# Kernel tuning notes

Hardware: AMD Instinct MI355X
Metric: run time of the kernel (lower is better)

Reference implementation:

```python
import jax, jax.numpy as jnp
import numpy as np

B, NP, NT = 16, 4096, 77
QD, CD, H, DH = 512, 768, 8, 64
INNER = H * DH


def setup_inputs() -> dict:
    key = jax.random.key(0)
    ks = jax.random.split(key, 8)
    s = 0.02
    return {
        "x": jax.random.normal(ks[0], (B, NP, QD), jnp.float32),
        "context": jax.random.normal(ks[1], (B, NT, CD), jnp.float32),
        "mask": jnp.ones((B, NP, NT), jnp.int32),
        "Wq": jax.random.normal(ks[2], (QD, INNER), jnp.float32) * s,
        "Wk": jax.random.normal(ks[3], (CD, INNER), jnp.float32) * s,
        "Wv": jax.random.normal(ks[4], (CD, INNER), jnp.float32) * s,
        "Wo": jax.random.normal(ks[5], (INNER, QD), jnp.float32) * s,
        "bo": jnp.zeros((QD,), jnp.float32),
    }


def reference(x, context, mask, Wq, Wk, Wv, Wo, bo):
    scale = 1.0 / jnp.sqrt(jnp.asarray(DH, x.dtype))
    # projections -> (B, H, N, DH)
    q = (x @ Wq).reshape(B, NP, H, DH).transpose(0, 2, 1, 3)
    k = (context @ Wk).reshape(B, NT, H, DH).transpose(0, 2, 1, 3)
    v = (context @ Wv).reshape(B, NT, H, DH).transpose(0, 2, 1, 3)
    # scores (B, H, NP, NT)
    attn = jnp.einsum("bhqd,bhkd->bhqk", q, k) * scale
    attn = jnp.where(mask[:, None, :, :] == 0, -jnp.inf, attn)
    attn = jax.nn.softmax(attn, axis=-1)
    out = jnp.einsum("bhqk,bhkd->bhqd", attn, v)
    out = out.transpose(0, 2, 1, 3).reshape(B, NP, INNER)
    return out @ Wo + bo
```

## Files before the change

kernel.cpp:

```cpp
#include <hip/hip_runtime.h>


typedef _Float16 half_t;
typedef _Float16 half8 __attribute__((ext_vector_type(8)));
typedef float f32x4 __attribute__((ext_vector_type(4)));
typedef unsigned int u32;

#define NB 16
#define NP 4096
#define NT 77
#define NTP 96
#define QD 512
#define CD 768
#define NH 8
#define DH 64
#define INNER 512
#define MKV (NB * NT)

__device__ __forceinline__ void stage16(const void* g, void* l) {
    __builtin_amdgcn_global_load_lds((const __attribute__((address_space(1))) u32*)g,
                                     (__attribute__((address_space(3))) u32*)l, 16, 0, 0);
}

__device__ __forceinline__ f32x4 mfma16(half8 a, half8 b, f32x4 c) {
    return __builtin_amdgcn_mfma_f32_16x16x32_f16(a, b, c, 0, 0, 0);
}

__global__ __launch_bounds__(256) void kTrans2(const float* __restrict__ in0,
                                               const float* __restrict__ in1,
                                               half_t* __restrict__ out0,
                                               half_t* __restrict__ out1,
                                               int K, int N) {
    const float* in = blockIdx.z ? in1 : in0;
    half_t* out = blockIdx.z ? out1 : out0;
    __shared__ float tile[32][33];
    int tx = threadIdx.x & 31, ty = threadIdx.x >> 5;
    int kb = blockIdx.y * 32, nb = blockIdx.x * 32;
    for (int r = ty; r < 32; r += 8)
        tile[r][tx] = in[(size_t)(kb + r) * N + nb + tx];
    __syncthreads();
    for (int r = ty; r < 32; r += 8)
        out[(size_t)(nb + r) * K + kb + tx] = (half_t)tile[tx][r];
}

__global__ __launch_bounds__(256) void kKVproj(const float* __restrict__ Ctx,
                                               const half_t* __restrict__ WkT,
                                               const half_t* __restrict__ WvT,
                                               half_t* __restrict__ Kp,
                                               half_t* __restrict__ VTp) {
    __shared__ alignas(16) half_t As[64 * 64];
    __shared__ alignas(16) half_t Bs[128 * 64];
    const int t = threadIdx.x, w = t >> 6, lane = t & 63;
    const int c0 = lane & 15, q4 = lane >> 4;
    const int rx = c0 & 7;
    const int m0 = blockIdx.y * 64;
    const int n0g = blockIdx.x * 128;
    const int z = n0g >= 512;
    const int n0 = n0g - z * 512;
    const half_t* WT = z ? WvT : WkT;

    f32x4 acc[4][2] = {};
    for (int k0 = 0; k0 < CD; k0 += 64) {
        for (int q = 0; q < 2; ++q) {
            int c = q * 256 + t;
            int row = c >> 3, ch = c & 7;
            int gr = m0 + row; if (gr > MKV - 1) gr = MKV - 1;
            const float* src = Ctx + (size_t)gr * CD + k0 + ch * 8;
            f32x4 f0 = *(const f32x4*)src;
            f32x4 f1 = *(const f32x4*)(src + 4);
            half8 hv;
            for (int e = 0; e < 4; ++e) { hv[e] = (half_t)f0[e]; hv[4 + e] = (half_t)f1[e]; }
            *(half8*)&As[row * 64 + ((ch ^ (row & 7)) * 8)] = hv;
        }
        for (int q = 0; q < 4; ++q) {
            int c = q * 256 + t;
            int row = c >> 3, k8 = c & 7;
            stage16(WT + (size_t)(n0 + row) * CD + k0 + (k8 ^ (row & 7)) * 8, &Bs[c * 8]);
        }
        __syncthreads();
        for (int ks = 0; ks < 2; ++ks) {
            int ch = ks * 4 + q4;
            int cx = (ch ^ rx) * 8;
            half8 a[4], b[2];
            for (int i = 0; i < 4; ++i)
                a[i] = *(const half8*)&As[(16 * i + c0) * 64 + cx];
            for (int j = 0; j < 2; ++j)
                b[j] = *(const half8*)&Bs[(w * 32 + 16 * j + c0) * 64 + cx];
            for (int i = 0; i < 4; ++i)
                for (int j = 0; j < 2; ++j)
                    acc[i][j] = mfma16(a[i], b[j], acc[i][j]);
        }
        __syncthreads();
    }
    for (int i = 0; i < 4; ++i)
        for (int j = 0; j < 2; ++j)
            for (int r = 0; r < 4; ++r) {
                int row = m0 + 16 * i + q4 * 4 + r;
                if (row >= MKV) continue;
                int col = n0 + w * 32 + 16 * j + c0;
                int b = row / NT, tt = row - b * NT;
                int h = col >> 6, d = col & 63;
                half_t v = (half_t)acc[i][j][r];
                if (!z) Kp[(((size_t)b * NH + h) * NTP + tt) * DH + d] = v;
                else    VTp[(((size_t)b * NH + h) * DH + d) * NTP + tt] = v;
            }
}

__global__ __launch_bounds__(256) void kQproj(const float* __restrict__ X,
                                              const half_t* __restrict__ WqT,
                                              half_t* __restrict__ Q) {
    __shared__ alignas(16) half_t As[128 * 64];
    __shared__ alignas(16) half_t Bs[128 * 64];
    const int t = threadIdx.x, w = t >> 6, lane = t & 63;
    const int c0 = lane & 15, q4 = lane >> 4;
    const int rx = c0 & 7;
    const int wm = w & 1, wn = w >> 1;
    const int bid = blockIdx.x;
    const int wid = (bid & 7) * 256 + (bid >> 3);
    const int m0 = (wid >> 2) * 128, n0 = (wid & 3) * 128;

    f32x4 acc[4][4] = {};
    for (int k0 = 0; k0 < QD; k0 += 64) {
        for (int q = 0; q < 4; ++q) {
            int c = q * 256 + t;
            int row = c >> 3, ch = c & 7;
            const float* src = X + (size_t)(m0 + row) * QD + k0 + ch * 8;
            f32x4 f0 = *(const f32x4*)src;
            f32x4 f1 = *(const f32x4*)(src + 4);
            half8 hv;
            for (int e = 0; e < 4; ++e) { hv[e] = (half_t)f0[e]; hv[4 + e] = (half_t)f1[e]; }
            *(half8*)&As[row * 64 + ((ch ^ (row & 7)) * 8)] = hv;
        }
        for (int q = 0; q < 4; ++q) {
            int c = q * 256 + t;
            int row = c >> 3, k8 = c & 7;
            stage16(WqT + (size_t)(n0 + row) * QD + k0 + (k8 ^ (row & 7)) * 8, &Bs[c * 8]);
        }
        __syncthreads();
        for (int ks = 0; ks < 2; ++ks) {
            int cx = ((ks * 4 + q4) ^ rx) * 8;
            half8 a[4];
            for (int i = 0; i < 4; ++i)
                a[i] = *(const half8*)&As[(wm * 64 + 16 * i + c0) * 64 + cx];
            for (int j = 0; j < 4; ++j) {
                half8 bv = *(const half8*)&Bs[(wn * 64 + 16 * j + c0) * 64 + cx];
                for (int i = 0; i < 4; ++i)
                    acc[i][j] = mfma16(a[i], bv, acc[i][j]);
            }
        }
        __syncthreads();
    }
    for (int i = 0; i < 4; ++i)
        for (int j = 0; j < 4; ++j)
            for (int r = 0; r < 4; ++r) {
                int row = m0 + wm * 64 + 16 * i + q4 * 4 + r;
                int col = n0 + wn * 64 + 16 * j + c0;
                Q[(size_t)row * INNER + col] = (half_t)acc[i][j][r];
            }
}

__global__ __launch_bounds__(256) void kAttn(half_t* __restrict__ Q,
                                             const half_t* __restrict__ Kp,
                                             const half_t* __restrict__ VTp,
                                             const int* __restrict__ mask) {
    __shared__ alignas(16) half_t Qs[128 * 104];
    __shared__ alignas(16) half_t Ks[NTP * 72];
    __shared__ alignas(16) half_t VTs[DH * 104];
    const int t = threadIdx.x, w = t >> 6, lane = t & 63;
    const int c0 = lane & 15, q4 = lane >> 4;
    const int qt = blockIdx.x, h = blockIdx.y, b = blockIdx.z;
    const int q0 = qt * 128;
    const size_t qbase = ((size_t)b * NP + q0) * INNER + h * DH;

    for (int q = 0; q < 4; ++q) {
        int c = q * 256 + t, m = c >> 3, k8 = (c & 7) * 8;
        *(uint4*)&Qs[m * 104 + k8] = *(const uint4*)(Q + qbase + (size_t)m * INNER + k8);
    }
    const half_t* Kh = Kp + ((size_t)b * NH + h) * NTP * DH;
    for (int q = 0; q < 3; ++q) {
        int c = q * 256 + t, r = c >> 3, k8 = (c & 7) * 8;
        *(uint4*)&Ks[r * 72 + k8] = *(const uint4*)(Kh + r * DH + k8);
    }
    const half_t* Vh = VTp + ((size_t)b * NH + h) * DH * NTP;
    for (int q = 0; q < 3; ++q) {
        int c = q * 256 + t, r = c / 12, t8 = (c % 12) * 8;
        *(uint4*)&VTs[r * 104 + t8] = *(const uint4*)(Vh + r * NTP + t8);
    }
    __syncthreads();

    const int r0 = w * 32;
    f32x4 sacc[2][6] = {};
    for (int ks = 0; ks < 2; ++ks) {
        half8 a0 = *(const half8*)&Qs[(r0 + c0) * 104 + ks * 32 + q4 * 8];
        half8 a1 = *(const half8*)&Qs[(r0 + 16 + c0) * 104 + ks * 32 + q4 * 8];
        for (int j = 0; j < 6; ++j) {
            half8 bv = *(const half8*)&Ks[(16 * j + c0) * 72 + ks * 32 + q4 * 8];
            sacc[0][j] = mfma16(a0, bv, sacc[0][j]);
            sacc[1][j] = mfma16(a1, bv, sacc[1][j]);
        }
    }

    for (int i = 0; i < 2; ++i)
        for (int r = 0; r < 4; ++r) {
            int qrow = r0 + 16 * i + q4 * 4 + r;
            const int* mrow = mask + ((size_t)b * NP + q0 + qrow) * NT;
            float sv[6];
            for (int j = 0; j < 6; ++j) {
                int tt = 16 * j + c0;
                float s = sacc[i][j][r] * 0.125f;
                bool valid = (tt < NT) && (mrow[tt < NT ? tt : NT - 1] != 0);
                sv[j] = valid ? s : -1e30f;
            }
            float mx = sv[0];
            for (int j = 1; j < 6; ++j) mx = fmaxf(mx, sv[j]);
            for (int d = 1; d < 16; d <<= 1) mx = fmaxf(mx, __shfl_xor(mx, d));
            float pv[6], sum = 0.f;
            for (int j = 0; j < 6; ++j) { pv[j] = __expf(sv[j] - mx); sum += pv[j]; }
            for (int d = 1; d < 16; d <<= 1) sum += __shfl_xor(sum, d);
            float inv = 1.0f / sum;
            for (int j = 0; j < 6; ++j)
                Qs[qrow * 104 + 16 * j + c0] = (half_t)(pv[j] * inv);
        }

    f32x4 oacc[2][4] = {};
    for (int ks = 0; ks < 3; ++ks) {
        half8 a0 = *(const half8*)&Qs[(r0 + c0) * 104 + ks * 32 + q4 * 8];
        half8 a1 = *(const half8*)&Qs[(r0 + 16 + c0) * 104 + ks * 32 + q4 * 8];
        for (int j = 0; j < 4; ++j) {
            half8 bv = *(const half8*)&VTs[(16 * j + c0) * 104 + ks * 32 + q4 * 8];
            oacc[0][j] = mfma16(a0, bv, oacc[0][j]);
            oacc[1][j] = mfma16(a1, bv, oacc[1][j]);
        }
    }
    for (int i = 0; i < 2; ++i)
        for (int j = 0; j < 4; ++j)
            for (int r = 0; r < 4; ++r) {
                int qrow = r0 + 16 * i + q4 * 4 + r;
                int d = 16 * j + c0;
                Q[qbase + (size_t)qrow * INNER + d] = (half_t)oacc[2 > 1 ? i : i][j][r];
            }
}

__global__ __launch_bounds__(256) void kOproj(const half_t* __restrict__ AO,
                                              const half_t* __restrict__ WoT,
                                              const float* __restrict__ bo,
                                              float* __restrict__ out) {
    __shared__ alignas(16) half_t As[128 * 64];
    __shared__ alignas(16) half_t Bs[128 * 64];
    const int t = threadIdx.x, w = t >> 6, lane = t & 63;
    const int c0 = lane & 15, q4 = lane >> 4;
    const int rx = c0 & 7;
    const int wm = w & 1, wn = w >> 1;
    const int bid = blockIdx.x;
    const int wid = (bid & 7) * 256 + (bid >> 3);
    const int m0 = (wid >> 2) * 128, n0 = (wid & 3) * 128;

    float bj[4];
    for (int j = 0; j < 4; ++j) bj[j] = bo[n0 + wn * 64 + 16 * j + c0];

    f32x4 acc[4][4] = {};
    for (int k0 = 0; k0 < INNER; k0 += 64) {
        for (int q = 0; q < 4; ++q) {
            int c = q * 256 + t;
            int row = c >> 3, k8 = c & 7;
            stage16(AO + (size_t)(m0 + row) * INNER + k0 + (k8 ^ (row & 7)) * 8, &As[c * 8]);
        }
        for (int q = 0; q < 4; ++q) {
            int c = q * 256 + t;
            int row = c >> 3, k8 = c & 7;
            stage16(WoT + (size_t)(n0 + row) * INNER + k0 + (k8 ^ (row & 7)) * 8, &Bs[c * 8]);
        }
        __syncthreads();
        for (int ks = 0; ks < 2; ++ks) {
            int cx = ((ks * 4 + q4) ^ rx) * 8;
            half8 a[4];
            for (int i = 0; i < 4; ++i)
                a[i] = *(const half8*)&As[(wm * 64 + 16 * i + c0) * 64 + cx];
            for (int j = 0; j < 4; ++j) {
                half8 bv = *(const half8*)&Bs[(wn * 64 + 16 * j + c0) * 64 + cx];
                for (int i = 0; i < 4; ++i)
                    acc[i][j] = mfma16(a[i], bv, acc[i][j]);
            }
        }
        __syncthreads();
    }
    for (int i = 0; i < 4; ++i)
        for (int j = 0; j < 4; ++j)
            for (int r = 0; r < 4; ++r) {
                int row = m0 + wm * 64 + 16 * i + q4 * 4 + r;
                int col = n0 + wn * 64 + 16 * j + c0;
                out[(size_t)row * QD + col] = acc[i][j][r] + bj[j];
            }
}

extern "C" void kernel_launch(void* const* d_in, const int* in_sizes, int n_in,
                              void* d_out, int out_size, void* d_ws, size_t ws_size,
                              hipStream_t stream) {
    const float* x   = (const float*)d_in[0];
    const float* ctx = (const float*)d_in[1];
    const int*   msk = (const int*)d_in[2];
    const float* Wq  = (const float*)d_in[3];
    const float* Wk  = (const float*)d_in[4];
    const float* Wv  = (const float*)d_in[5];
    const float* Wo  = (const float*)d_in[6];
    const float* bo  = (const float*)d_in[7];
    float* out = (float*)d_out;

    half_t* Qws = (half_t*)d_ws;
    half_t* WqT = Qws + (size_t)NB * NP * INNER;
    half_t* WoT = WqT + (size_t)QD * INNER;
    half_t* WkT = WoT + (size_t)INNER * QD;
    half_t* WvT = WkT + (size_t)INNER * CD;
    half_t* Kp  = WvT + (size_t)INNER * CD;
    half_t* VTp = Kp + (size_t)NB * NH * NTP * DH;

    kTrans2<<<dim3(INNER / 32, QD / 32, 2), 256, 0, stream>>>(Wq, Wo, WqT, WoT, QD, INNER);
    kTrans2<<<dim3(INNER / 32, CD / 32, 2), 256, 0, stream>>>(Wk, Wv, WkT, WvT, CD, INNER);
    hipMemsetAsync(Kp, 0, (size_t)NB * NH * (NTP * DH + DH * NTP) * sizeof(half_t), stream);
    kKVproj<<<dim3(8, 20), 256, 0, stream>>>(ctx, WkT, WvT, Kp, VTp);
    kQproj<<<dim3(2048), 256, 0, stream>>>(x, WqT, Qws);
    kAttn<<<dim3(NP / 128, NH, NB), 256, 0, stream>>>(Qws, Kp, VTp, msk);
    kOproj<<<dim3(2048), 256, 0, stream>>>(Qws, WoT, bo, out);
}
```

Baseline: 407.4 us.

## Double-buffer LDS tiles in projection GEMMs and raise MFMA wave priority in attention

Converts the K/V, Q and output projection GEMMs to a double-buffered LDS pipeline. The next k-tile's global loads (register prefetch plus fp16 convert for the fp32 activations, direct-to-LDS for the weights) are issued before the MFMAs on the current tile, so load latency can overlap compute and only one barrier per iteration remains. It also wraps the attention kernel's MFMA loops in s_setprio to favor matrix-issuing waves. The cost is doubled LDS use (64 KB for the 128x128 GEMMs), which may lower occupancy, plus extra prefetch registers.

```diff
diff --git a/kernel.cpp b/kernel.cpp
--- a/kernel.cpp
+++ b/kernel.cpp
@@ -48,8 +48,8 @@
                                                const half_t* __restrict__ WvT,
                                                half_t* __restrict__ Kp,
                                                half_t* __restrict__ VTp) {
-    __shared__ alignas(16) half_t As[64 * 64];
-    __shared__ alignas(16) half_t Bs[128 * 64];
+    __shared__ alignas(16) half_t As[2][64 * 64];
+    __shared__ alignas(16) half_t Bs[2][128 * 64];
     const int t = threadIdx.x, w = t >> 6, lane = t & 63;
     const int c0 = lane & 15, q4 = lane >> 4;
     const int rx = c0 & 7;
@@ -59,38 +59,54 @@
     const int n0 = n0g - z * 512;
     const half_t* WT = z ? WvT : WkT;
 
-    f32x4 acc[4][2] = {};
-    for (int k0 = 0; k0 < CD; k0 += 64) {
+    f32x4 pf[2][2];
+    auto issueA = [&](int k0) {
         for (int q = 0; q < 2; ++q) {
             int c = q * 256 + t;
             int row = c >> 3, ch = c & 7;
             int gr = m0 + row; if (gr > MKV - 1) gr = MKV - 1;
             const float* src = Ctx + (size_t)gr * CD + k0 + ch * 8;
-            f32x4 f0 = *(const f32x4*)src;
-            f32x4 f1 = *(const f32x4*)(src + 4);
+            pf[q][0] = *(const f32x4*)src;
+            pf[q][1] = *(const f32x4*)(src + 4);
+        }
+    };
+    auto writeA = [&](half_t* dst) {
+        for (int q = 0; q < 2; ++q) {
+            int c = q * 256 + t;
+            int row = c >> 3, ch = c & 7;
             half8 hv;
-            for (int e = 0; e < 4; ++e) { hv[e] = (half_t)f0[e]; hv[4 + e] = (half_t)f1[e]; }
-            *(half8*)&As[row * 64 + ((ch ^ (row & 7)) * 8)] = hv;
-        }
+            for (int e = 0; e < 4; ++e) { hv[e] = (half_t)pf[q][0][e]; hv[4 + e] = (half_t)pf[q][1][e]; }
+            *(half8*)&dst[row * 64 + ((ch ^ (row & 7)) * 8)] = hv;
+        }
+    };
+    auto stageB = [&](int k0, half_t* dst) {
         for (int q = 0; q < 4; ++q) {
             int c = q * 256 + t;
             int row = c >> 3, k8 = c & 7;
-            stage16(WT + (size_t)(n0 + row) * CD + k0 + (k8 ^ (row & 7)) * 8, &Bs[c * 8]);
-        }
-        __syncthreads();
+            stage16(WT + (size_t)(n0 + row) * CD + k0 + (k8 ^ (row & 7)) * 8, &dst[c * 8]);
+        }
+    };
+
+    f32x4 acc[4][2] = {};
+    issueA(0); stageB(0, Bs[0]); writeA(As[0]);
+    __syncthreads();
+    int cb = 0;
+    for (int it = 0; it < 12; ++it) {
+        if (it < 11) { issueA((it + 1) * 64); stageB((it + 1) * 64, Bs[cb ^ 1]); }
         for (int ks = 0; ks < 2; ++ks) {
-            int ch = ks * 4 + q4;
-            int cx = (ch ^ rx) * 8;
+            int cx = ((ks * 4 + q4) ^ rx) * 8;
             half8 a[4], b[2];
             for (int i = 0; i < 4; ++i)
-                a[i] = *(const half8*)&As[(16 * i + c0) * 64 + cx];
+                a[i] = *(const half8*)&As[cb][(16 * i + c0) * 64 + cx];
             for (int j = 0; j < 2; ++j)
-                b[j] = *(const half8*)&Bs[(w * 32 + 16 * j + c0) * 64 + cx];
+                b[j] = *(const half8*)&Bs[cb][(w * 32 + 16 * j + c0) * 64 + cx];
             for (int i = 0; i < 4; ++i)
                 for (int j = 0; j < 2; ++j)
                     acc[i][j] = mfma16(a[i], b[j], acc[i][j]);
         }
+        if (it < 11) writeA(As[cb ^ 1]);
         __syncthreads();
+        cb ^= 1;
     }
     for (int i = 0; i < 4; ++i)
         for (int j = 0; j < 2; ++j)
@@ -109,8 +125,8 @@
 __global__ __launch_bounds__(256) void kQproj(const float* __restrict__ X,
                                               const half_t* __restrict__ WqT,
                                               half_t* __restrict__ Q) {
-    __shared__ alignas(16) half_t As[128 * 64];
-    __shared__ alignas(16) half_t Bs[128 * 64];
+    __shared__ alignas(16) half_t As[2][128 * 64];
+    __shared__ alignas(16) half_t Bs[2][128 * 64];
     const int t = threadIdx.x, w = t >> 6, lane = t & 63;
     const int c0 = lane & 15, q4 = lane >> 4;
     const int rx = c0 & 7;
@@ -119,36 +135,53 @@
     const int wid = (bid & 7) * 256 + (bid >> 3);
     const int m0 = (wid >> 2) * 128, n0 = (wid & 3) * 128;
 
-    f32x4 acc[4][4] = {};
-    for (int k0 = 0; k0 < QD; k0 += 64) {
+    f32x4 pf[4][2];
+    auto issueA = [&](int k0) {
         for (int q = 0; q < 4; ++q) {
             int c = q * 256 + t;
             int row = c >> 3, ch = c & 7;
             const float* src = X + (size_t)(m0 + row) * QD + k0 + ch * 8;
-            f32x4 f0 = *(const f32x4*)src;
-            f32x4 f1 = *(const f32x4*)(src + 4);
+            pf[q][0] = *(const f32x4*)src;
+            pf[q][1] = *(const f32x4*)(src + 4);
+        }
+    };
+    auto writeA = [&](half_t* dst) {
+        for (int q = 0; q < 4; ++q) {
+            int c = q * 256 + t;
+            int row = c >> 3, ch = c & 7;
             half8 hv;
-            for (int e = 0; e < 4; ++e) { hv[e] = (half_t)f0[e]; hv[4 + e] = (half_t)f1[e]; }
-            *(half8*)&As[row * 64 + ((ch ^ (row & 7)) * 8)] = hv;
-        }
+            for (int e = 0; e < 4; ++e) { hv[e] = (half_t)pf[q][0][e]; hv[4 + e] = (half_t)pf[q][1][e]; }
+            *(half8*)&dst[row * 64 + ((ch ^ (row & 7)) * 8)] = hv;
+        }
+    };
+    auto stageB = [&](int k0, half_t* dst) {
         for (int q = 0; q < 4; ++q) {
             int c = q * 256 + t;
             int row = c >> 3, k8 = c & 7;
-            stage16(WqT + (size_t)(n0 + row) * QD + k0 + (k8 ^ (row & 7)) * 8, &Bs[c * 8]);
-        }
-        __syncthreads();
+            stage16(WqT + (size_t)(n0 + row) * QD + k0 + (k8 ^ (row & 7)) * 8, &dst[c * 8]);
+        }
+    };
+
+    f32x4 acc[4][4] = {};
+    issueA(0); stageB(0, Bs[0]); writeA(As[0]);
+    __syncthreads();
+    int cb = 0;
+    for (int it = 0; it < 8; ++it) {
+        if (it < 7) { issueA((it + 1) * 64); stageB((it + 1) * 64, Bs[cb ^ 1]); }
         for (int ks = 0; ks < 2; ++ks) {
             int cx = ((ks * 4 + q4) ^ rx) * 8;
             half8 a[4];
             for (int i = 0; i < 4; ++i)
-                a[i] = *(const half8*)&As[(wm * 64 + 16 * i + c0) * 64 + cx];
+                a[i] = *(const half8*)&As[cb][(wm * 64 + 16 * i + c0) * 64 + cx];
             for (int j = 0; j < 4; ++j) {
-                half8 bv = *(const half8*)&Bs[(wn * 64 + 16 * j + c0) * 64 + cx];
+                half8 bv = *(const half8*)&Bs[cb][(wn * 64 + 16 * j + c0) * 64 + cx];
                 for (int i = 0; i < 4; ++i)
                     acc[i][j] = mfma16(a[i], bv, acc[i][j]);
             }
         }
+        if (it < 7) writeA(As[cb ^ 1]);
         __syncthreads();
+        cb ^= 1;
     }
     for (int i = 0; i < 4; ++i)
         for (int j = 0; j < 4; ++j)
@@ -190,6 +223,7 @@
 
     const int r0 = w * 32;
     f32x4 sacc[2][6] = {};
+    __builtin_amdgcn_s_setprio(1);
     for (int ks = 0; ks < 2; ++ks) {
         half8 a0 = *(const half8*)&Qs[(r0 + c0) * 104 + ks * 32 + q4 * 8];
         half8 a1 = *(const half8*)&Qs[(r0 + 16 + c0) * 104 + ks * 32 + q4 * 8];
@@ -199,6 +233,7 @@
             sacc[1][j] = mfma16(a1, bv, sacc[1][j]);
         }
     }
+    __builtin_amdgcn_s_setprio(0);
 
     for (int i = 0; i < 2; ++i)
         for (int r = 0; r < 4; ++r) {
@@ -223,6 +258,7 @@
         }
 
     f32x4 oacc[2][4] = {};
+    __builtin_amdgcn_s_setprio(1);
     for (int ks = 0; ks < 3; ++ks) {
         half8 a0 = *(const half8*)&Qs[(r0 + c0) * 104 + ks * 32 + q4 * 8];
         half8 a1 = *(const half8*)&Qs[(r0 + 16 + c0) * 104 + ks * 32 + q4 * 8];
@@ -232,12 +268,13 @@
             oacc[1][j] = mfma16(a1, bv, oacc[1][j]);
         }
     }
+    __builtin_amdgcn_s_setprio(0);
     for (int i = 0; i < 2; ++i)
         for (int j = 0; j < 4; ++j)
             for (int r = 0; r < 4; ++r) {
                 int qrow = r0 + 16 * i + q4 * 4 + r;
                 int d = 16 * j + c0;
-                Q[qbase + (size_t)qrow * INNER + d] = (half_t)oacc[2 > 1 ? i : i][j][r];
+                Q[qbase + (size_t)qrow * INNER + d] = (half_t)oacc[i][j][r];
             }
 }
 
@@ -245,8 +282,8 @@
                                               const half_t* __restrict__ WoT,
                                               const float* __restrict__ bo,
                                               float* __restrict__ out) {
-    __shared__ alignas(16) half_t As[128 * 64];
-    __shared__ alignas(16) half_t Bs[128 * 64];
+    __shared__ alignas(16) half_t As[2][128 * 64];
+    __shared__ alignas(16) half_t Bs[2][128 * 64];
     const int t = threadIdx.x, w = t >> 6, lane = t & 63;
     const int c0 = lane & 15, q4 = lane >> 4;
     const int rx = c0 & 7;
@@ -258,31 +295,38 @@
     float bj[4];
     for (int j = 0; j < 4; ++j) bj[j] = bo[n0 + wn * 64 + 16 * j + c0];
 
+    auto stageAB = [&](int k0, half_t* dA, half_t* dB) {
+        for (int q = 0; q < 4; ++q) {
+            int c = q * 256 + t;
+            int row = c >> 3, k8 = c & 7;
+            stage16(AO + (size_t)(m0 + row) * INNER + k0 + (k8 ^ (row & 7)) * 8, &dA[c * 8]);
+        }
+        for (int q = 0; q < 4; ++q) {
+            int c = q * 256 + t;
+            int row = c >> 3, k8 = c & 7;
+            stage16(WoT + (size_t)(n0 + row) * INNER + k0 + (k8 ^ (row & 7)) * 8, &dB[c * 8]);
+        }
+    };
+
     f32x4 acc[4][4] = {};
-    for (int k0 = 0; k0 < INNER; k0 += 64) {
-        for (int q = 0; q < 4; ++q) {
-            int c = q * 256 + t;
-            int row = c >> 3, k8 = c & 7;
-            stage16(AO + (size_t)(m0 + row) * INNER + k0 + (k8 ^ (row & 7)) * 8, &As[c * 8]);
-        }
-        for (int q = 0; q < 4; ++q) {
-            int c = q * 256 + t;
-            int row = c >> 3, k8 = c & 7;
-            stage16(WoT + (size_t)(n0 + row) * INNER + k0 + (k8 ^ (row & 7)) * 8, &Bs[c * 8]);
-        }
-        __syncthreads();
+    stageAB(0, As[0], Bs[0]);
+    __syncthreads();
+    int cb = 0;
+    for (int it = 0; it < 8; ++it) {
+        if (it < 7) stageAB((it + 1) * 64, As[cb ^ 1], Bs[cb ^ 1]);
         for (int ks = 0; ks < 2; ++ks) {
             int cx = ((ks * 4 + q4) ^ rx) * 8;
             half8 a[4];
             for (int i = 0; i < 4; ++i)
-                a[i] = *(const half8*)&As[(wm * 64 + 16 * i + c0) * 64 + cx];
+                a[i] = *(const half8*)&As[cb][(wm * 64 + 16 * i + c0) * 64 + cx];
             for (int j = 0; j < 4; ++j) {
-                half8 bv = *(const half8*)&Bs[(wn * 64 + 16 * j + c0) * 64 + cx];
+                half8 bv = *(const half8*)&Bs[cb][(wn * 64 + 16 * j + c0) * 64 + cx];
                 for (int i = 0; i < 4; ++i)
                     acc[i][j] = mfma16(a[i], bv, acc[i][j]);
             }
         }
         __syncthreads();
+        cb ^= 1;
     }
     for (int i = 0; i < 4; ++i)
         for (int j = 0; j < 4; ++j)
```

New measurement: 435.0 us. +6.8%, slower.

## Prefetch A tiles into registers one step ahead in Q and O projection GEMMs

Applied to the files above, without the earlier changes.

The Q and O projection GEMMs now load the next A tile into registers while the current tile is consumed by MFMAs, then write it to shared memory after a barrier. In the O projection this replaces direct global-to-LDS staging of A with register loads. The aim is to hide global load latency behind compute, at the cost of more registers and an extra barrier per iteration. The attention kernel also raises wave priority around its MFMA loops via s_setprio.

```diff
diff --git a/kernel.cpp b/kernel.cpp
--- a/kernel.cpp
+++ b/kernel.cpp
@@ -79,8 +79,7 @@
         }
         __syncthreads();
         for (int ks = 0; ks < 2; ++ks) {
-            int ch = ks * 4 + q4;
-            int cx = (ch ^ rx) * 8;
+            int cx = ((ks * 4 + q4) ^ rx) * 8;
             half8 a[4], b[2];
             for (int i = 0; i < 4; ++i)
                 a[i] = *(const half8*)&As[(16 * i + c0) * 64 + cx];
@@ -119,24 +118,40 @@
     const int wid = (bid & 7) * 256 + (bid >> 3);
     const int m0 = (wid >> 2) * 128, n0 = (wid & 3) * 128;
 
-    f32x4 acc[4][4] = {};
-    for (int k0 = 0; k0 < QD; k0 += 64) {
+    f32x4 pa[4][2];
+    auto issueA = [&](int k0) {
         for (int q = 0; q < 4; ++q) {
             int c = q * 256 + t;
             int row = c >> 3, ch = c & 7;
             const float* src = X + (size_t)(m0 + row) * QD + k0 + ch * 8;
-            f32x4 f0 = *(const f32x4*)src;
-            f32x4 f1 = *(const f32x4*)(src + 4);
+            pa[q][0] = *(const f32x4*)src;
+            pa[q][1] = *(const f32x4*)(src + 4);
+        }
+    };
+    auto writeA = [&]() {
+        for (int q = 0; q < 4; ++q) {
+            int c = q * 256 + t;
+            int row = c >> 3, ch = c & 7;
             half8 hv;
-            for (int e = 0; e < 4; ++e) { hv[e] = (half_t)f0[e]; hv[4 + e] = (half_t)f1[e]; }
+            for (int e = 0; e < 4; ++e) { hv[e] = (half_t)pa[q][0][e]; hv[4 + e] = (half_t)pa[q][1][e]; }
             *(half8*)&As[row * 64 + ((ch ^ (row & 7)) * 8)] = hv;
         }
+    };
+    auto stageB = [&](int k0) {
         for (int q = 0; q < 4; ++q) {
             int c = q * 256 + t;
             int row = c >> 3, k8 = c & 7;
             stage16(WqT + (size_t)(n0 + row) * QD + k0 + (k8 ^ (row & 7)) * 8, &Bs[c * 8]);
         }
-        __syncthreads();
+    };
+
+    f32x4 acc[4][4] = {};
+    issueA(0);
+    stageB(0);
+    writeA();
+    __syncthreads();
+    issueA(64);
+    for (int it = 0; it < 8; ++it) {
         for (int ks = 0; ks < 2; ++ks) {
             int cx = ((ks * 4 + q4) ^ rx) * 8;
             half8 a[4];
@@ -148,7 +163,13 @@
                     acc[i][j] = mfma16(a[i], bv, acc[i][j]);
             }
         }
-        __syncthreads();
+        if (it < 7) {
+            __syncthreads();
+            writeA();
+            stageB((it + 1) * 64);
+            if (it < 6) issueA((it + 2) * 64);
+            __syncthreads();
+        }
     }
     for (int i = 0; i < 4; ++i)
         for (int j = 0; j < 4; ++j)
@@ -190,6 +211,7 @@
 
     const int r0 = w * 32;
     f32x4 sacc[2][6] = {};
+    __builtin_amdgcn_s_setprio(1);
     for (int ks = 0; ks < 2; ++ks) {
         half8 a0 = *(const half8*)&Qs[(r0 + c0) * 104 + ks * 32 + q4 * 8];
         half8 a1 = *(const half8*)&Qs[(r0 + 16 + c0) * 104 + ks * 32 + q4 * 8];
@@ -199,6 +221,7 @@
             sacc[1][j] = mfma16(a1, bv, sacc[1][j]);
         }
     }
+    __builtin_amdgcn_s_setprio(0);
 
     for (int i = 0; i < 2; ++i)
         for (int r = 0; r < 4; ++r) {
@@ -223,6 +246,7 @@
         }
 
     f32x4 oacc[2][4] = {};
+    __builtin_amdgcn_s_setprio(1);
     for (int ks = 0; ks < 3; ++ks) {
         half8 a0 = *(const half8*)&Qs[(r0 + c0) * 104 + ks * 32 + q4 * 8];
         half8 a1 = *(const half8*)&Qs[(r0 + 16 + c0) * 104 + ks * 32 + q4 * 8];
@@ -232,12 +256,13 @@
             oacc[1][j] = mfma16(a1, bv, oacc[1][j]);
         }
     }
+    __builtin_amdgcn_s_setprio(0);
     for (int i = 0; i < 2; ++i)
         for (int j = 0; j < 4; ++j)
             for (int r = 0; r < 4; ++r) {
                 int qrow = r0 + 16 * i + q4 * 4 + r;
                 int d = 16 * j + c0;
-                Q[qbase + (size_t)qrow * INNER + d] = (half_t)oacc[2 > 1 ? i : i][j][r];
+                Q[qbase + (size_t)qrow * INNER + d] = (half_t)oacc[i][j][r];
             }
 }
 
@@ -258,19 +283,36 @@
     float bj[4];
     for (int j = 0; j < 4; ++j) bj[j] = bo[n0 + wn * 64 + 16 * j + c0];
 
-    f32x4 acc[4][4] = {};
-    for (int k0 = 0; k0 < INNER; k0 += 64) {
-        for (int q = 0; q < 4; ++q) {
-            int c = q * 256 + t;
-            int row = c >> 3, k8 = c & 7;
-            stage16(AO + (size_t)(m0 + row) * INNER + k0 + (k8 ^ (row & 7)) * 8, &As[c * 8]);
-        }
+    uint4 pa[4];
+    auto issueA = [&](int k0) {
+        for (int q = 0; q < 4; ++q) {
+            int c = q * 256 + t;
+            int row = c >> 3, ch = c & 7;
+            pa[q] = *(const uint4*)(AO + (size_t)(m0 + row) * INNER + k0 + ch * 8);
+        }
+    };
+    auto writeA = [&]() {
+        for (int q = 0; q < 4; ++q) {
+            int c = q * 256 + t;
+            int row = c >> 3, ch = c & 7;
+            *(uint4*)&As[row * 64 + ((ch ^ (row & 7)) * 8)] = pa[q];
+        }
+    };
+    auto stageB = [&](int k0) {
         for (int q = 0; q < 4; ++q) {
             int c = q * 256 + t;
             int row = c >> 3, k8 = c & 7;
             stage16(WoT + (size_t)(n0 + row) * INNER + k0 + (k8 ^ (row & 7)) * 8, &Bs[c * 8]);
         }
-        __syncthreads();
+    };
+
+    f32x4 acc[4][4] = {};
+    issueA(0);
+    stageB(0);
+    writeA();
+    __syncthreads();
+    issueA(64);
+    for (int it = 0; it < 8; ++it) {
         for (int ks = 0; ks < 2; ++ks) {
             int cx = ((ks * 4 + q4) ^ rx) * 8;
             half8 a[4];
@@ -282,7 +324,13 @@
                     acc[i][j] = mfma16(a[i], bv, acc[i][j]);
             }
         }
-        __syncthreads();
+        if (it < 7) {
+            __syncthreads();
+            writeA();
+            stageB((it + 1) * 64);
+            if (it < 6) issueA((it + 2) * 64);
+            __syncthreads();
+        }
     }
     for (int i = 0; i < 4; ++i)
         for (int j = 0; j < 4; ++j)
```

New measurement: 480.0 us. 17.8% more time.
